# Optimization experiments

Hardware: AMD Instinct MI355X
Metric: run time of the kernel (lower is better)

Reference implementation:

```python
import jax, jax.numpy as jnp
import numpy as np

RANK = 4
ALPHA = 32
SCALING = ALPHA / RANK  # 8.0
LORA_STRENGTH = 1.0


def setup_inputs() -> dict:
    key = jax.random.key(0)
    ks = jax.random.split(key, 7)
    d_out, d_in = 4096, 4096  # Mistral q/k/v/o_proj weight shape
    batch, seq = 1, 512
    x = jax.random.normal(ks[0], (batch, seq, d_in), dtype=jnp.float32)
    W = jax.random.normal(ks[1], (d_out, d_in), dtype=jnp.float32) * 0.02  # frozen base weight
    A = jax.random.normal(ks[2], (d_out, RANK), dtype=jnp.float32)
    B = jax.random.normal(ks[3], (RANK, d_in), dtype=jnp.float32)
    zc_w = jax.random.normal(ks[4], (), dtype=jnp.float32)  # Conv2d(1,1,1) weight (scalar)
    zc_b = jax.random.normal(ks[5], (), dtype=jnp.float32)  # Conv2d(1,1,1) bias (scalar)
    bias = jax.random.normal(ks[6], (d_out,), dtype=jnp.float32)
    return {"x": x, "W": W, "A": A, "B": B, "zc_w": zc_w, "zc_b": zc_b, "bias": bias}


def reference(x, W, A, B, zc_w, zc_b, bias):
    # low_rank_update = scaling * (A @ B), then 1x1 zero-conv = elementwise scale + bias
    low = SCALING * jnp.einsum('or,ri->oi', A, B)          # [d_out, d_in]
    low = zc_w * low + zc_b                                 # zero_conv (scalar affine)
    W_prime = LORA_STRENGTH * W + low                       # [d_out, d_in]
    # x @ W_prime.T + bias
    return jnp.einsum('bsi,oi->bso', x, W_prime) + bias
```

## Files before the change

kernel.cpp:

```cpp
#include <hip/hip_runtime.h>
#include <hip/hip_bf16.h>


typedef __attribute__((ext_vector_type(8))) short bf16x8;
typedef __attribute__((ext_vector_type(4))) short bf16x4;
typedef __attribute__((ext_vector_type(4))) unsigned short u16x4;
typedef __attribute__((ext_vector_type(4))) float f32x4;

#define MDIM 512
#define NDIM 4096
#define KDIM 4096
#define BM 128
#define BN 128
#define BK 64
#define NT (KDIM / BK)

#define VMCNT(n) asm volatile("s_waitcnt vmcnt(" #n ")" ::: "memory")
#define LGKM0()  asm volatile("s_waitcnt lgkmcnt(0)" ::: "memory")

static __device__ inline unsigned short f2bf(float f) {
  return __bfloat16_as_ushort(__float2bfloat16(f));
}

static __device__ inline void gll16(const void* g, void* l) {
  __builtin_amdgcn_global_load_lds(
      (const __attribute__((address_space(1))) void*)g,
      (__attribute__((address_space(3))) void*)l, 16, 0, 0);
}

__global__ __launch_bounds__(256) void tk_kernel(
    const float* __restrict__ x, const float* __restrict__ B,
    float* __restrict__ t, float* __restrict__ xs,
    unsigned short* __restrict__ xbf) {
  const int tid = threadIdx.x;
  const int s = blockIdx.x;
  const float* xr = x + (long)s * KDIM;
  float a0 = 0.f, a1 = 0.f, a2 = 0.f, a3 = 0.f, a4 = 0.f;
  for (int k = tid * 4; k < KDIM; k += 1024) {
    f32x4 xv = *(const f32x4*)&xr[k];
    if (xbf) {
      bf16x4 bv;
      bv[0] = (short)f2bf(xv[0]); bv[1] = (short)f2bf(xv[1]);
      bv[2] = (short)f2bf(xv[2]); bv[3] = (short)f2bf(xv[3]);
      *(bf16x4*)&xbf[(long)s * KDIM + k] = bv;
    }
    f32x4 b0 = *(const f32x4*)&B[0 * KDIM + k];
    f32x4 b1 = *(const f32x4*)&B[1 * KDIM + k];
    f32x4 b2 = *(const f32x4*)&B[2 * KDIM + k];
    f32x4 b3 = *(const f32x4*)&B[3 * KDIM + k];
    a0 += xv[0]*b0[0] + xv[1]*b0[1] + xv[2]*b0[2] + xv[3]*b0[3];
    a1 += xv[0]*b1[0] + xv[1]*b1[1] + xv[2]*b1[2] + xv[3]*b1[3];
    a2 += xv[0]*b2[0] + xv[1]*b2[1] + xv[2]*b2[2] + xv[3]*b2[3];
    a3 += xv[0]*b3[0] + xv[1]*b3[1] + xv[2]*b3[2] + xv[3]*b3[3];
    a4 += xv[0] + xv[1] + xv[2] + xv[3];
  }
  #pragma unroll
  for (int off = 32; off; off >>= 1) {
    a0 += __shfl_down(a0, off, 64);
    a1 += __shfl_down(a1, off, 64);
    a2 += __shfl_down(a2, off, 64);
    a3 += __shfl_down(a3, off, 64);
    a4 += __shfl_down(a4, off, 64);
  }
  __shared__ float red[4][5];
  int w = tid >> 6, l = tid & 63;
  if (l == 0) { red[w][0]=a0; red[w][1]=a1; red[w][2]=a2; red[w][3]=a3; red[w][4]=a4; }
  __syncthreads();
  if (tid == 0) {
    t[0 * MDIM + s] = red[0][0] + red[1][0] + red[2][0] + red[3][0];
    t[1 * MDIM + s] = red[0][1] + red[1][1] + red[2][1] + red[3][1];
    t[2 * MDIM + s] = red[0][2] + red[1][2] + red[2][2] + red[3][2];
    t[3 * MDIM + s] = red[0][3] + red[1][3] + red[2][3] + red[3][3];
    xs[s]           = red[0][4] + red[1][4] + red[2][4] + red[3][4];
  }
}

template<int NSPLIT, bool FUSED>
__global__ __launch_bounds__(256, 2) void gemm_hyb(
    const unsigned short* __restrict__ xb, const float* __restrict__ W,
    const float* __restrict__ A, const float* __restrict__ bias,
    const float* __restrict__ zcw, const float* __restrict__ zcb,
    const float* __restrict__ t, const float* __restrict__ xs,
    float* __restrict__ dst) {
  __shared__ __align__(16) unsigned short As[2][BM * BK];
  __shared__ __align__(16) unsigned short Ws[2][BN * BK];

  const int bm = blockIdx.x >> 5;
  const int bn = blockIdx.x & 31;
  const int ks = blockIdx.y;
  const int NTloc = NT / NSPLIT;
  const int kbase = ks * (KDIM / NSPLIT);

  const int tid = threadIdx.x;
  const int lane = tid & 63;
  const int wv = tid >> 6;
  const int wm = wv >> 1;
  const int wn = wv & 1;

  const int srow8 = lane >> 3;
  const int schk = (lane & 7) ^ srow8;
  const unsigned short* xsrc[4];
  #pragma unroll
  for (int i = 0; i < 4; ++i) {
    const int row = i * 32 + wv * 8 + srow8;
    xsrc[i] = xb + (long)(bm * BM + row) * KDIM + kbase + schk * 8;
  }
  auto XSTAGE = [&](int kt) {
    const int koff = kt * BK;
    const int slot = kt & 1;
    #pragma unroll
    for (int i = 0; i < 4; ++i)
      gll16(xsrc[i] + koff, &As[slot][i * 2048 + wv * 512]);
  };

  const float* wgp = W + (long)(bn * BN + wv * 32 + (lane >> 4)) * KDIM
                       + kbase + (lane & 15) * 4;
  f32x4 wrE[8], wrO[8];
  auto WISSUE = [&](f32x4 (&wr)[8], int kt) {
    #pragma unroll
    for (int i = 0; i < 8; ++i)
      wr[i] = *(const f32x4*)(wgp + (long)i * 4 * KDIM + kt * BK);
  };
  auto WWRITE = [&](const f32x4 (&wr)[8], int slot) {
    #pragma unroll
    for (int i = 0; i < 8; ++i) {
      const int r = wv * 32 + (lane >> 4) + i * 4;
      const int idx = r * 64 + (((((lane & 15) >> 1)) ^ (r & 7)) << 3) + (lane & 1) * 4;
      u16x4 v;
      v[0] = f2bf(wr[i][0]); v[1] = f2bf(wr[i][1]);
      v[2] = f2bf(wr[i][2]); v[3] = f2bf(wr[i][3]);
      *(u16x4*)&Ws[slot][idx] = v;
    }
  };

  const int fr = lane & 15;
  const int q = lane >> 4;
  const int frs = fr & 7;

  f32x4 acc[4][4] = {};

  auto COMPUTE = [&](int slot) {
    #pragma unroll
    for (int kseg = 0; kseg < 2; ++kseg) {
      const int c = ((kseg * 4 + q) ^ frs) * 8;
      bf16x8 af[4], bf[4];
      #pragma unroll
      for (int mi = 0; mi < 4; ++mi)
        af[mi] = *(const bf16x8*)&As[slot][(wm * 64 + mi * 16 + fr) * BK + c];
      #pragma unroll
      for (int ni = 0; ni < 4; ++ni)
        bf[ni] = *(const bf16x8*)&Ws[slot][(wn * 64 + ni * 16 + fr) * BK + c];
      __builtin_amdgcn_s_setprio(1);
      #pragma unroll
      for (int mi = 0; mi < 4; ++mi)
        #pragma unroll
        for (int ni = 0; ni < 4; ++ni)
          acc[mi][ni] = __builtin_amdgcn_mfma_f32_16x16x32_bf16(
              af[mi], bf[ni], acc[mi][ni], 0, 0, 0);
      __builtin_amdgcn_s_setprio(0);
    }
  };

  WISSUE(wrE, 0);
  XSTAGE(0);
  __builtin_amdgcn_sched_barrier(0);
  WISSUE(wrO, 1);
  __builtin_amdgcn_sched_barrier(0);
  WWRITE(wrE, 0);
  VMCNT(8);
  LGKM0();
  __builtin_amdgcn_s_barrier();
  __builtin_amdgcn_sched_barrier(0);

  #define BODY(KT, WRISS, WRCON)                                   \
    do {                                                           \
      XSTAGE((KT) + 1);                                            \
      __builtin_amdgcn_sched_barrier(0);                           \
      WISSUE(WRISS, (KT) + 2);                                     \
      COMPUTE((KT) & 1);                                           \
      WWRITE(WRCON, ((KT) + 1) & 1);                               \
      VMCNT(8);                                                    \
      LGKM0();                                                     \
      __builtin_amdgcn_s_barrier();                                \
      __builtin_amdgcn_sched_barrier(0);                           \
    } while (0)

  for (int kt = 0; kt < NTloc - 2; kt += 2) {
    BODY(kt, wrE, wrO);
    BODY(kt + 1, wrO, wrE);
  }
  XSTAGE(NTloc - 1);
  __builtin_amdgcn_sched_barrier(0);
  COMPUTE((NTloc - 2) & 1);
  WWRITE(wrO, (NTloc - 1) & 1);
  VMCNT(0);
  LGKM0();
  __builtin_amdgcn_s_barrier();
  __builtin_amdgcn_sched_barrier(0);
  COMPUTE((NTloc - 1) & 1);
  #undef BODY

  const int s0 = bm * BM + wm * 64;
  const int o0 = bn * BN + wn * 64;
  if (FUSED) {
    const float zw8 = zcw[0] * 8.0f;
    const float zb = zcb[0];
    #pragma unroll
    for (int mi = 0; mi < 4; ++mi) {
      const int sb = s0 + mi * 16 + q * 4;
      f32x4 t0 = *(const f32x4*)&t[0 * MDIM + sb];
      f32x4 t1 = *(const f32x4*)&t[1 * MDIM + sb];
      f32x4 t2 = *(const f32x4*)&t[2 * MDIM + sb];
      f32x4 t3 = *(const f32x4*)&t[3 * MDIM + sb];
      f32x4 x4 = *(const f32x4*)&xs[sb];
      #pragma unroll
      for (int ni = 0; ni < 4; ++ni) {
        const int o = o0 + ni * 16 + fr;
        f32x4 a4 = *(const f32x4*)&A[o * 4];
        const float bo = bias[o];
        #pragma unroll
        for (int j = 0; j < 4; ++j) {
          float corr = zw8 * (a4[0] * t0[j] + a4[1] * t1[j] + a4[2] * t2[j] + a4[3] * t3[j])
                     + zb * x4[j] + bo;
          dst[(long)(sb + j) * NDIM + o] = acc[mi][ni][j] + corr;
        }
      }
    }
  } else {
    float* p = dst + (size_t)ks * MDIM * NDIM;
    #pragma unroll
    for (int mi = 0; mi < 4; ++mi) {
      const int sb = s0 + mi * 16 + q * 4;
      #pragma unroll
      for (int ni = 0; ni < 4; ++ni) {
        const int o = o0 + ni * 16 + fr;
        #pragma unroll
        for (int j = 0; j < 4; ++j)
          p[(long)(sb + j) * NDIM + o] = acc[mi][ni][j];
      }
    }
  }
}

__global__ __launch_bounds__(256) void reduce_kernel(
    const float* __restrict__ p,
    const float* __restrict__ A, const float* __restrict__ bias,
    const float* __restrict__ zcw, const float* __restrict__ zcb,
    const float* __restrict__ t, const float* __restrict__ xs,
    float* __restrict__ out) {
  const long base = ((long)blockIdx.x * 256 + threadIdx.x) * 4;
  const int s = (int)(base / NDIM);
  const int o = (int)(base % NDIM);
  f32x4 v0 = *(const f32x4*)&p[base];
  f32x4 v1 = *(const f32x4*)&p[(long)MDIM * NDIM + base];
  f32x4 v2 = *(const f32x4*)&p[(long)2 * MDIM * NDIM + base];
  f32x4 v3 = *(const f32x4*)&p[(long)3 * MDIM * NDIM + base];
  const float zw8 = zcw[0] * 8.0f;
  const float zb = zcb[0];
  const float t0 = t[0 * MDIM + s], t1 = t[1 * MDIM + s];
  const float t2 = t[2 * MDIM + s], t3 = t[3 * MDIM + s];
  const float xv = xs[s];
  f32x4 bo = *(const f32x4*)&bias[o];
  f32x4 r;
  #pragma unroll
  for (int j = 0; j < 4; ++j) {
    f32x4 a4 = *(const f32x4*)&A[(o + j) * 4];
    r[j] = (v0[j] + v1[j]) + (v2[j] + v3[j])
         + zw8 * (a4[0] * t0 + a4[1] * t1 + a4[2] * t2 + a4[3] * t3)
         + zb * xv + bo[j];
  }
  *(f32x4*)&out[base] = r;
}

__global__ __launch_bounds__(256) void gemm_fallback(
    const float* __restrict__ x, const float* __restrict__ W,
    const float* __restrict__ A, const float* __restrict__ bias,
    const float* __restrict__ zcw, const float* __restrict__ zcb,
    const float* __restrict__ t, const float* __restrict__ xs,
    float* __restrict__ out) {
  __shared__ __align__(16) unsigned short Asf[2][64 * 64];
  __shared__ __align__(16) unsigned short Wsf[2][64 * 64];
  const int bid = blockIdx.x;
  const int bn = bid & 63, bm = bid >> 6;
  const int tid = threadIdx.x, lane = tid & 63, wid = tid >> 6;
  const int wm = wid >> 1, wn = wid & 1;
  const int srow = tid >> 2, sc0 = (tid & 3) * 16;
  const float* xg = x + (long)(bm * 64 + srow) * KDIM + sc0;
  const float* wg = W + (long)(bn * 64 + srow) * KDIM + sc0;
  const int off0 = (srow * 64 + sc0) ^ ((srow & 7) << 3);
  const int off1 = (srow * 64 + sc0 + 8) ^ ((srow & 7) << 3);
  const int fr = lane & 15, fk = (lane >> 4) * 8;
  f32x4 acc[2][2] = {};
  f32x4 xv0, xv1, xv2, xv3, wv0, wv1, wv2, wv3;
  auto pk8 = [](f32x4 a, f32x4 b) {
    bf16x8 v;
    v[0] = (short)f2bf(a[0]); v[1] = (short)f2bf(a[1]);
    v[2] = (short)f2bf(a[2]); v[3] = (short)f2bf(a[3]);
    v[4] = (short)f2bf(b[0]); v[5] = (short)f2bf(b[1]);
    v[6] = (short)f2bf(b[2]); v[7] = (short)f2bf(b[3]);
    return v;
  };
  xv0 = *(const f32x4*)(xg);      xv1 = *(const f32x4*)(xg + 4);
  xv2 = *(const f32x4*)(xg + 8);  xv3 = *(const f32x4*)(xg + 12);
  wv0 = *(const f32x4*)(wg);      wv1 = *(const f32x4*)(wg + 4);
  wv2 = *(const f32x4*)(wg + 8);  wv3 = *(const f32x4*)(wg + 12);
  *(bf16x8*)&Asf[0][off0] = pk8(xv0, xv1);
  *(bf16x8*)&Asf[0][off1] = pk8(xv2, xv3);
  *(bf16x8*)&Wsf[0][off0] = pk8(wv0, wv1);
  *(bf16x8*)&Wsf[0][off1] = pk8(wv2, wv3);
  __syncthreads();
  for (int kt = 0; kt < NT; ++kt) {
    const int cur = kt & 1;
    if (kt + 1 < NT) {
      const int off = (kt + 1) * 64;
      xv0 = *(const f32x4*)(xg + off);      xv1 = *(const f32x4*)(xg + off + 4);
      xv2 = *(const f32x4*)(xg + off + 8);  xv3 = *(const f32x4*)(xg + off + 12);
      wv0 = *(const f32x4*)(wg + off);      wv1 = *(const f32x4*)(wg + off + 4);
      wv2 = *(const f32x4*)(wg + off + 8);  wv3 = *(const f32x4*)(wg + off + 12);
    }
    #pragma unroll
    for (int kss = 0; kss < 2; ++kss) {
      const int kk = kss * 32 + fk;
      const int ra0 = wm * 32 + fr, ra1 = ra0 + 16;
      const int rb0 = wn * 32 + fr, rb1 = rb0 + 16;
      bf16x8 a0 = *(const bf16x8*)&Asf[cur][(ra0 * 64 + kk) ^ ((ra0 & 7) << 3)];
      bf16x8 a1 = *(const bf16x8*)&Asf[cur][(ra1 * 64 + kk) ^ ((ra1 & 7) << 3)];
      bf16x8 b0 = *(const bf16x8*)&Wsf[cur][(rb0 * 64 + kk) ^ ((rb0 & 7) << 3)];
      bf16x8 b1 = *(const bf16x8*)&Wsf[cur][(rb1 * 64 + kk) ^ ((rb1 & 7) << 3)];
      acc[0][0] = __builtin_amdgcn_mfma_f32_16x16x32_bf16(a0, b0, acc[0][0], 0, 0, 0);
      acc[0][1] = __builtin_amdgcn_mfma_f32_16x16x32_bf16(a0, b1, acc[0][1], 0, 0, 0);
      acc[1][0] = __builtin_amdgcn_mfma_f32_16x16x32_bf16(a1, b0, acc[1][0], 0, 0, 0);
      acc[1][1] = __builtin_amdgcn_mfma_f32_16x16x32_bf16(a1, b1, acc[1][1], 0, 0, 0);
    }
    if (kt + 1 < NT) {
      const int nxt = cur ^ 1;
      *(bf16x8*)&Asf[nxt][off0] = pk8(xv0, xv1);
      *(bf16x8*)&Asf[nxt][off1] = pk8(xv2, xv3);
      *(bf16x8*)&Wsf[nxt][off0] = pk8(wv0, wv1);
      *(bf16x8*)&Wsf[nxt][off1] = pk8(wv2, wv3);
    }
    __syncthreads();
  }
  const float zw8 = zcw[0] * 8.0f;
  const float zb = zcb[0];
  const int s0 = bm * 64 + wm * 32;
  const int o0 = bn * 64 + wn * 32;
  #pragma unroll
  for (int mi = 0; mi < 2; ++mi) {
    const int sb = s0 + mi * 16 + ((lane >> 4) * 4);
    f32x4 t0 = *(const f32x4*)&t[0 * MDIM + sb];
    f32x4 t1 = *(const f32x4*)&t[1 * MDIM + sb];
    f32x4 t2 = *(const f32x4*)&t[2 * MDIM + sb];
    f32x4 t3 = *(const f32x4*)&t[3 * MDIM + sb];
    f32x4 x4 = *(const f32x4*)&xs[sb];
    #pragma unroll
    for (int ni = 0; ni < 2; ++ni) {
      const int o = o0 + ni * 16 + fr;
      f32x4 a4 = *(const f32x4*)&A[o * 4];
      const float bo = bias[o];
      #pragma unroll
      for (int j = 0; j < 4; ++j) {
        float corr = zw8 * (a4[0] * t0[j] + a4[1] * t1[j] + a4[2] * t2[j] + a4[3] * t3[j])
                   + zb * x4[j] + bo;
        out[(long)(sb + j) * NDIM + o] = acc[mi][ni][j] + corr;
      }
    }
  }
}

extern "C" void kernel_launch(void* const* d_in, const int* in_sizes, int n_in,
                              void* d_out, int out_size, void* d_ws, size_t ws_size,
                              hipStream_t stream) {
  const float* x    = (const float*)d_in[0];
  const float* W    = (const float*)d_in[1];
  const float* A    = (const float*)d_in[2];
  const float* B    = (const float*)d_in[3];
  const float* zcw  = (const float*)d_in[4];
  const float* zcb  = (const float*)d_in[5];
  const float* bias = (const float*)d_in[6];
  float* out = (float*)d_out;

  float* t  = (float*)d_ws;
  float* xs = t + 4 * MDIM;
  unsigned short* xbf = (unsigned short*)(t + 4096);
  float* pbuf = (float*)(xbf + (size_t)MDIM * KDIM);

  const size_t need_x = 4096u * 4 + (size_t)MDIM * KDIM * 2;
  const size_t need_p = need_x + (size_t)4 * MDIM * NDIM * 4;

  if (ws_size >= need_p) {
    tk_kernel<<<MDIM, 256, 0, stream>>>(x, B, t, xs, xbf);
    gemm_hyb<4, false><<<dim3(4 * 32, 4), 256, 0, stream>>>(
        xbf, W, A, bias, zcw, zcb, t, xs, pbuf);
    reduce_kernel<<<(MDIM * NDIM) / (4 * 256), 256, 0, stream>>>(
        pbuf, A, bias, zcw, zcb, t, xs, out);
  } else if (ws_size >= need_x) {
    tk_kernel<<<MDIM, 256, 0, stream>>>(x, B, t, xs, xbf);
    gemm_hyb<1, true><<<dim3(4 * 32, 1), 256, 0, stream>>>(
        xbf, W, A, bias, zcw, zcb, t, xs, out);
  } else {
    tk_kernel<<<MDIM, 256, 0, stream>>>(x, B, t, xs, nullptr);
    gemm_fallback<<<(MDIM / 64) * (NDIM / 64), 256, 0, stream>>>(
        x, W, A, bias, zcw, zcb, t, xs, out);
  }
}
```

Baseline: 46.46 us.

## Feed W fragments straight from registers and triple-buffer x tiles in LDS

The GEMM no longer stages the converted W tile through LDS. Each wave loads its 32 W rows directly into registers in MFMA fragment layout, converts them to bf16 and uses them as the B operand, so every wave covers all 128 rows of M against its own 32 output columns. The x tile is now triple-buffered with async global-to-LDS loads, which leaves a single barrier per k-step and removes the LDS write and lgkm waits for W. The cost is more x LDS reads per wave (8 A fragments instead of 4), a larger accumulator (8x2), and W global latency now sits directly in front of the convert step. The min-blocks-per-CU launch bound is also dropped.

```diff
diff --git a/kernel.cpp b/kernel.cpp
--- a/kernel.cpp
+++ b/kernel.cpp
@@ -4,7 +4,6 @@
 
 typedef __attribute__((ext_vector_type(8))) short bf16x8;
 typedef __attribute__((ext_vector_type(4))) short bf16x4;
-typedef __attribute__((ext_vector_type(4))) unsigned short u16x4;
 typedef __attribute__((ext_vector_type(4))) float f32x4;
 
 #define MDIM 512
@@ -16,10 +15,18 @@
 #define NT (KDIM / BK)
 
 #define VMCNT(n) asm volatile("s_waitcnt vmcnt(" #n ")" ::: "memory")
-#define LGKM0()  asm volatile("s_waitcnt lgkmcnt(0)" ::: "memory")
 
 static __device__ inline unsigned short f2bf(float f) {
   return __bfloat16_as_ushort(__float2bfloat16(f));
+}
+
+static __device__ inline bf16x8 pack8(f32x4 a, f32x4 b) {
+  bf16x8 v;
+  v[0] = (short)f2bf(a[0]); v[1] = (short)f2bf(a[1]);
+  v[2] = (short)f2bf(a[2]); v[3] = (short)f2bf(a[3]);
+  v[4] = (short)f2bf(b[0]); v[5] = (short)f2bf(b[1]);
+  v[6] = (short)f2bf(b[2]); v[7] = (short)f2bf(b[3]);
+  return v;
 }
 
 static __device__ inline void gll16(const void* g, void* l) {
@@ -76,14 +83,13 @@
 }
 
 template<int NSPLIT, bool FUSED>
-__global__ __launch_bounds__(256, 2) void gemm_hyb(
+__global__ __launch_bounds__(256) void gemm_wr(
     const unsigned short* __restrict__ xb, const float* __restrict__ W,
     const float* __restrict__ A, const float* __restrict__ bias,
     const float* __restrict__ zcw, const float* __restrict__ zcb,
     const float* __restrict__ t, const float* __restrict__ xs,
     float* __restrict__ dst) {
-  __shared__ __align__(16) unsigned short As[2][BM * BK];
-  __shared__ __align__(16) unsigned short Ws[2][BN * BK];
+  __shared__ __align__(16) unsigned short As[3][BM * BK];
 
   const int bm = blockIdx.x >> 5;
   const int bn = blockIdx.x & 31;
@@ -94,8 +100,6 @@
   const int tid = threadIdx.x;
   const int lane = tid & 63;
   const int wv = tid >> 6;
-  const int wm = wv >> 1;
-  const int wn = wv & 1;
 
   const int srow8 = lane >> 3;
   const int schk = (lane & 7) ^ srow8;
@@ -105,108 +109,92 @@
     const int row = i * 32 + wv * 8 + srow8;
     xsrc[i] = xb + (long)(bm * BM + row) * KDIM + kbase + schk * 8;
   }
-  auto XSTAGE = [&](int kt) {
+  auto XSTAGE = [&](int kt, int slot) {
     const int koff = kt * BK;
-    const int slot = kt & 1;
     #pragma unroll
     for (int i = 0; i < 4; ++i)
       gll16(xsrc[i] + koff, &As[slot][i * 2048 + wv * 512]);
   };
 
-  const float* wgp = W + (long)(bn * BN + wv * 32 + (lane >> 4)) * KDIM
-                       + kbase + (lane & 15) * 4;
-  f32x4 wrE[8], wrO[8];
-  auto WISSUE = [&](f32x4 (&wr)[8], int kt) {
-    #pragma unroll
-    for (int i = 0; i < 8; ++i)
-      wr[i] = *(const f32x4*)(wgp + (long)i * 4 * KDIM + kt * BK);
-  };
-  auto WWRITE = [&](const f32x4 (&wr)[8], int slot) {
-    #pragma unroll
-    for (int i = 0; i < 8; ++i) {
-      const int r = wv * 32 + (lane >> 4) + i * 4;
-      const int idx = r * 64 + (((((lane & 15) >> 1)) ^ (r & 7)) << 3) + (lane & 1) * 4;
-      u16x4 v;
-      v[0] = f2bf(wr[i][0]); v[1] = f2bf(wr[i][1]);
-      v[2] = f2bf(wr[i][2]); v[3] = f2bf(wr[i][3]);
-      *(u16x4*)&Ws[slot][idx] = v;
-    }
-  };
-
   const int fr = lane & 15;
   const int q = lane >> 4;
   const int frs = fr & 7;
-
-  f32x4 acc[4][4] = {};
+  const float* wp0 = W + (long)(bn * BN + wv * 32 + fr) * KDIM + kbase + q * 8;
+  const float* wp1 = wp0 + (long)16 * KDIM;
+
+  f32x4 w32[2][2][2];
+  bf16x8 wb[2][2];
+
+  auto WLOAD = [&](int kt) {
+    const int koff = kt * BK;
+    #pragma unroll
+    for (int kseg = 0; kseg < 2; ++kseg) {
+      #pragma unroll
+      for (int h = 0; h < 2; ++h) {
+        w32[0][kseg][h] = *(const f32x4*)(wp0 + koff + kseg * 32 + h * 4);
+        w32[1][kseg][h] = *(const f32x4*)(wp1 + koff + kseg * 32 + h * 4);
+      }
+    }
+  };
+  auto WCVT = [&]() {
+    #pragma unroll
+    for (int ni = 0; ni < 2; ++ni)
+      #pragma unroll
+      for (int kseg = 0; kseg < 2; ++kseg)
+        wb[ni][kseg] = pack8(w32[ni][kseg][0], w32[ni][kseg][1]);
+  };
+
+  f32x4 acc[8][2] = {};
 
   auto COMPUTE = [&](int slot) {
     #pragma unroll
     for (int kseg = 0; kseg < 2; ++kseg) {
       const int c = ((kseg * 4 + q) ^ frs) * 8;
-      bf16x8 af[4], bf[4];
-      #pragma unroll
-      for (int mi = 0; mi < 4; ++mi)
-        af[mi] = *(const bf16x8*)&As[slot][(wm * 64 + mi * 16 + fr) * BK + c];
-      #pragma unroll
-      for (int ni = 0; ni < 4; ++ni)
-        bf[ni] = *(const bf16x8*)&Ws[slot][(wn * 64 + ni * 16 + fr) * BK + c];
+      bf16x8 af[8];
+      #pragma unroll
+      for (int mi = 0; mi < 8; ++mi)
+        af[mi] = *(const bf16x8*)&As[slot][(mi * 16 + fr) * BK + c];
       __builtin_amdgcn_s_setprio(1);
       #pragma unroll
-      for (int mi = 0; mi < 4; ++mi)
-        #pragma unroll
-        for (int ni = 0; ni < 4; ++ni)
-          acc[mi][ni] = __builtin_amdgcn_mfma_f32_16x16x32_bf16(
-              af[mi], bf[ni], acc[mi][ni], 0, 0, 0);
+      for (int mi = 0; mi < 8; ++mi) {
+        acc[mi][0] = __builtin_amdgcn_mfma_f32_16x16x32_bf16(
+            af[mi], wb[0][kseg], acc[mi][0], 0, 0, 0);
+        acc[mi][1] = __builtin_amdgcn_mfma_f32_16x16x32_bf16(
+            af[mi], wb[1][kseg], acc[mi][1], 0, 0, 0);
+      }
       __builtin_amdgcn_s_setprio(0);
     }
   };
 
-  WISSUE(wrE, 0);
-  XSTAGE(0);
+  XSTAGE(0, 0);
+  XSTAGE(1, 1);
   __builtin_amdgcn_sched_barrier(0);
-  WISSUE(wrO, 1);
-  __builtin_amdgcn_sched_barrier(0);
-  WWRITE(wrE, 0);
+  WLOAD(0);
   VMCNT(8);
-  LGKM0();
   __builtin_amdgcn_s_barrier();
   __builtin_amdgcn_sched_barrier(0);
 
-  #define BODY(KT, WRISS, WRCON)                                   \
-    do {                                                           \
-      XSTAGE((KT) + 1);                                            \
-      __builtin_amdgcn_sched_barrier(0);                           \
-      WISSUE(WRISS, (KT) + 2);                                     \
-      COMPUTE((KT) & 1);                                           \
-      WWRITE(WRCON, ((KT) + 1) & 1);                               \
-      VMCNT(8);                                                    \
-      LGKM0();                                                     \
-      __builtin_amdgcn_s_barrier();                                \
-      __builtin_amdgcn_sched_barrier(0);                           \
-    } while (0)
-
-  for (int kt = 0; kt < NTloc - 2; kt += 2) {
-    BODY(kt, wrE, wrO);
-    BODY(kt + 1, wrO, wrE);
-  }
-  XSTAGE(NTloc - 1);
-  __builtin_amdgcn_sched_barrier(0);
-  COMPUTE((NTloc - 2) & 1);
-  WWRITE(wrO, (NTloc - 1) & 1);
-  VMCNT(0);
-  LGKM0();
-  __builtin_amdgcn_s_barrier();
-  __builtin_amdgcn_sched_barrier(0);
-  COMPUTE((NTloc - 1) & 1);
-  #undef BODY
-
-  const int s0 = bm * BM + wm * 64;
-  const int o0 = bn * BN + wn * 64;
+  int sl_stage = 2;
+  int sl_comp = 0;
+  for (int kt = 0; kt < NTloc; ++kt) {
+    WCVT();
+    if (kt + 2 < NTloc) XSTAGE(kt + 2, sl_stage);
+    if (kt + 1 < NTloc) WLOAD(kt + 1);
+    __builtin_amdgcn_sched_barrier(0);
+    COMPUTE(sl_comp);
+    __builtin_amdgcn_s_barrier();
+    __builtin_amdgcn_sched_barrier(0);
+    sl_stage = (sl_stage == 2) ? 0 : sl_stage + 1;
+    sl_comp  = (sl_comp == 2) ? 0 : sl_comp + 1;
+  }
+
+  const int s0 = bm * BM;
+  const int o0 = bn * BN + wv * 32;
   if (FUSED) {
     const float zw8 = zcw[0] * 8.0f;
     const float zb = zcb[0];
     #pragma unroll
-    for (int mi = 0; mi < 4; ++mi) {
+    for (int mi = 0; mi < 8; ++mi) {
       const int sb = s0 + mi * 16 + q * 4;
       f32x4 t0 = *(const f32x4*)&t[0 * MDIM + sb];
       f32x4 t1 = *(const f32x4*)&t[1 * MDIM + sb];
@@ -214,7 +202,7 @@
       f32x4 t3 = *(const f32x4*)&t[3 * MDIM + sb];
       f32x4 x4 = *(const f32x4*)&xs[sb];
       #pragma unroll
-      for (int ni = 0; ni < 4; ++ni) {
+      for (int ni = 0; ni < 2; ++ni) {
         const int o = o0 + ni * 16 + fr;
         f32x4 a4 = *(const f32x4*)&A[o * 4];
         const float bo = bias[o];
@@ -229,10 +217,10 @@
   } else {
     float* p = dst + (size_t)ks * MDIM * NDIM;
     #pragma unroll
-    for (int mi = 0; mi < 4; ++mi) {
+    for (int mi = 0; mi < 8; ++mi) {
       const int sb = s0 + mi * 16 + q * 4;
       #pragma unroll
-      for (int ni = 0; ni < 4; ++ni) {
+      for (int ni = 0; ni < 2; ++ni) {
         const int o = o0 + ni * 16 + fr;
         #pragma unroll
         for (int j = 0; j < 4; ++j)
@@ -292,22 +280,14 @@
   const int fr = lane & 15, fk = (lane >> 4) * 8;
   f32x4 acc[2][2] = {};
   f32x4 xv0, xv1, xv2, xv3, wv0, wv1, wv2, wv3;
-  auto pk8 = [](f32x4 a, f32x4 b) {
-    bf16x8 v;
-    v[0] = (short)f2bf(a[0]); v[1] = (short)f2bf(a[1]);
-    v[2] = (short)f2bf(a[2]); v[3] = (short)f2bf(a[3]);
-    v[4] = (short)f2bf(b[0]); v[5] = (short)f2bf(b[1]);
-    v[6] = (short)f2bf(b[2]); v[7] = (short)f2bf(b[3]);
-    return v;
-  };
   xv0 = *(const f32x4*)(xg);      xv1 = *(const f32x4*)(xg + 4);
   xv2 = *(const f32x4*)(xg + 8);  xv3 = *(const f32x4*)(xg + 12);
   wv0 = *(const f32x4*)(wg);      wv1 = *(const f32x4*)(wg + 4);
   wv2 = *(const f32x4*)(wg + 8);  wv3 = *(const f32x4*)(wg + 12);
-  *(bf16x8*)&Asf[0][off0] = pk8(xv0, xv1);
-  *(bf16x8*)&Asf[0][off1] = pk8(xv2, xv3);
-  *(bf16x8*)&Wsf[0][off0] = pk8(wv0, wv1);
-  *(bf16x8*)&Wsf[0][off1] = pk8(wv2, wv3);
+  *(bf16x8*)&Asf[0][off0] = pack8(xv0, xv1);
+  *(bf16x8*)&Asf[0][off1] = pack8(xv2, xv3);
+  *(bf16x8*)&Wsf[0][off0] = pack8(wv0, wv1);
+  *(bf16x8*)&Wsf[0][off1] = pack8(wv2, wv3);
   __syncthreads();
   for (int kt = 0; kt < NT; ++kt) {
     const int cur = kt & 1;
@@ -334,10 +314,10 @@
     }
     if (kt + 1 < NT) {
       const int nxt = cur ^ 1;
-      *(bf16x8*)&Asf[nxt][off0] = pk8(xv0, xv1);
-      *(bf16x8*)&Asf[nxt][off1] = pk8(xv2, xv3);
-      *(bf16x8*)&Wsf[nxt][off0] = pk8(wv0, wv1);
-      *(bf16x8*)&Wsf[nxt][off1] = pk8(wv2, wv3);
+      *(bf16x8*)&Asf[nxt][off0] = pack8(xv0, xv1);
+      *(bf16x8*)&Asf[nxt][off1] = pack8(xv2, xv3);
+      *(bf16x8*)&Wsf[nxt][off0] = pack8(wv0, wv1);
+      *(bf16x8*)&Wsf[nxt][off1] = pack8(wv2, wv3);
     }
     __syncthreads();
   }
@@ -390,13 +370,13 @@
 
   if (ws_size >= need_p) {
     tk_kernel<<<MDIM, 256, 0, stream>>>(x, B, t, xs, xbf);
-    gemm_hyb<4, false><<<dim3(4 * 32, 4), 256, 0, stream>>>(
+    gemm_wr<4, false><<<dim3(4 * 32, 4), 256, 0, stream>>>(
         xbf, W, A, bias, zcw, zcb, t, xs, pbuf);
     reduce_kernel<<<(MDIM * NDIM) / (4 * 256), 256, 0, stream>>>(
         pbuf, A, bias, zcw, zcb, t, xs, out);
   } else if (ws_size >= need_x) {
     tk_kernel<<<MDIM, 256, 0, stream>>>(x, B, t, xs, xbf);
-    gemm_hyb<1, true><<<dim3(4 * 32, 1), 256, 0, stream>>>(
+    gemm_wr<1, true><<<dim3(4 * 32, 1), 256, 0, stream>>>(
         xbf, W, A, bias, zcw, zcb, t, xs, out);
   } else {
     tk_kernel<<<MDIM, 256, 0, stream>>>(x, B, t, xs, nullptr);
```

New measurement: 58.78 us. 26.5% more time.
